# Performance work log

Hardware: AMD Instinct MI355X
Metric: run time of the kernel (lower is better)

Reference implementation:

```python
import jax, jax.numpy as jnp
import numpy as np

B, C, N = 8, 512, 8192
H = 8
D = C // H
HID = int(C * 2.0)
EPS_ATTN = 1e-6
EPS_BN = 1e-5


def setup_inputs() -> dict:
    key = jax.random.key(0)
    ks = jax.random.split(key, 8)
    sc = lambda fan_in: 1.0 / np.sqrt(fan_in)
    return {
        "x": jax.random.normal(ks[0], (B, C, N), dtype=jnp.float32),
        # qkv Linear: stored [in, out] for x @ W
        "qkv_w": jax.random.normal(ks[1], (C, 3 * C), dtype=jnp.float32) * sc(C),
        "qkv_b": jnp.zeros((3 * C,), dtype=jnp.float32),
        "proj_w": jax.random.normal(ks[2], (C, C), dtype=jnp.float32) * sc(C),
        "proj_b": jnp.zeros((C,), dtype=jnp.float32),
        # FFN conv1x1 (no bias, BN follows)
        "w1": jax.random.normal(ks[3], (HID, C), dtype=jnp.float32) * sc(C),
        "g1": jnp.ones((HID,), dtype=jnp.float32),
        "b1": jnp.zeros((HID,), dtype=jnp.float32),
        "w2": jax.random.normal(ks[4], (C, HID), dtype=jnp.float32) * sc(HID),
        "g2": jnp.ones((C,), dtype=jnp.float32),
        "b2": jnp.zeros((C,), dtype=jnp.float32),
    }


def _phi(x):
    # elu(x) + 1  (strictly positive kernel feature map)
    return jax.nn.elu(x) + 1.0


def _bn(x, gamma, beta):
    # training-mode BatchNorm1d over [B, C, N]: stats over (batch, spatial)
    mean = jnp.mean(x, axis=(0, 2), keepdims=True)
    var = jnp.var(x, axis=(0, 2), keepdims=True)
    xh = (x - mean) * jax.lax.rsqrt(var + EPS_BN)
    return xh * gamma[None, :, None] + beta[None, :, None]


def reference(x, qkv_w, qkv_b, proj_w, proj_b, w1, g1, b1, w2, g2, b2):
    # ---- linear attention ----
    xt = jnp.swapaxes(x, 1, 2)                       # [B, N, C]
    qkv = xt @ qkv_w + qkv_b                         # [B, N, 3C]
    q, k, v = jnp.split(qkv, 3, axis=-1)
    reshape_h = lambda t: jnp.swapaxes(t.reshape(B, N, H, D), 1, 2)  # [B, H, N, D]
    q, k, v = reshape_h(q), reshape_h(k), reshape_h(v)
    q_phi = _phi(q)
    k_phi = _phi(k)
    S = jnp.einsum("bhnd,bhne->bhde", k_phi, v)      # K^T V, [B,H,D,D]
    k_sum = k_phi.sum(axis=-2)                       # [B,H,D]
    numer = jnp.einsum("bhnd,bhde->bhne", q_phi, S)  # [B,H,N,D]
    denom = jnp.einsum("bhnd,bhd->bhn", q_phi, k_sum)[..., None] + EPS_ATTN
    out = numer / denom                              # [B,H,N,D]
    out = jnp.swapaxes(out, 1, 2).reshape(B, N, C)
    out = out @ proj_w + proj_b                      # [B, N, C]
    y = jnp.swapaxes(out, 1, 2)                      # [B, C, N]
    # ---- attention residual ----
    x = x + y
    # ---- FFN: conv1x1 -> BN -> ReLU, twice ----
    h = jnp.einsum("oc,bcn->bon", w1, x)             # [B, HID, N]
    h = jax.nn.relu(_bn(h, g1, b1))
    h = jnp.einsum("oc,bcn->bon", w2, h)             # [B, C, N]
    h = jax.nn.relu(_bn(h, g2, b2))
    return x + h
```

## Files before the change

kernel.cpp:

```cpp
#include <hip/hip_runtime.h>
#include <hip/hip_bf16.h>

#define B_    8
#define C_    512
#define N_    8192
#define H_    8
#define D_    64
#define HID_  1024

constexpr float EPS_ATTN = 1e-6f;
constexpr float EPS_BN   = 1e-5f;

typedef _Float16 half8 __attribute__((ext_vector_type(8)));
typedef _Float16 half4 __attribute__((ext_vector_type(4)));
typedef float    floatx4 __attribute__((ext_vector_type(4)));

#define GLOAD_LDS(gp, lp) \
  __builtin_amdgcn_global_load_lds((const __attribute__((address_space(1))) void*)(gp), \
                                   (__attribute__((address_space(3))) void*)(lp), 16, 0, 0)

template<int EPI>
__global__ __launch_bounds__(256)
void gemm_mfma(const _Float16* __restrict__ Abase, size_t a_bstride,
               const _Float16* __restrict__ Wt, int K,
               float* __restrict__ OUTf, size_t outf_bs,
               _Float16* __restrict__ OUTh, size_t outh_bs,
               const float* __restrict__ bias,
               const float* __restrict__ resid, size_t res_bs,
               int phi_limit)
{
    __shared__ _Float16 Al[4096];
    __shared__ _Float16 Bl[4096];

    const int tid = threadIdx.x;
    const int b = blockIdx.z;
    const int n_base = blockIdx.x * 128;
    const int o_base = blockIdx.y * 128;
    const int w = tid >> 6, l = tid & 63;
    const int wm = w >> 1, wn = w & 1;

    const _Float16* A  = Abase + (size_t)b * a_bstride + (size_t)n_base * K;
    const _Float16* Bw = Wt + (size_t)o_base * K;

    const int r0 = tid & 127;
    const int s0 = tid >> 7;
    const _Float16* ga0 = A  + (size_t)r0 * K + s0 * 8;
    const _Float16* ga1 = A  + (size_t)r0 * K + (2 + s0) * 8;
    const _Float16* gb0 = Bw + (size_t)r0 * K + s0 * 8;
    const _Float16* gb1 = Bw + (size_t)r0 * K + (2 + s0) * 8;
    _Float16* la0 = &Al[(size_t)(tid & 192) * 8];
    _Float16* la1 = &Al[(size_t)(256 + (tid & 192)) * 8];
    _Float16* lb0 = &Bl[(size_t)(tid & 192) * 8];
    _Float16* lb1 = &Bl[(size_t)(256 + (tid & 192)) * 8];

    floatx4 acc[4][4];
    #pragma unroll
    for (int mi = 0; mi < 4; ++mi)
        #pragma unroll
        for (int ni = 0; ni < 4; ++ni)
            acc[mi][ni] = (floatx4){0.f, 0.f, 0.f, 0.f};

    const int s = l >> 4;
    const int r = l & 15;

    for (int c0 = 0; c0 < K; c0 += 32) {
        GLOAD_LDS(ga0 + c0, la0);
        GLOAD_LDS(ga1 + c0, la1);
        GLOAD_LDS(gb0 + c0, lb0);
        GLOAD_LDS(gb1 + c0, lb1);
        __syncthreads();
        half8 af[4], bf[4];
        #pragma unroll
        for (int f = 0; f < 4; ++f) {
            af[f] = *(const half8*)&Al[(size_t)(s * 128 + wm * 64 + f * 16 + r) * 8];
            bf[f] = *(const half8*)&Bl[(size_t)(s * 128 + wn * 64 + f * 16 + r) * 8];
        }
        #pragma unroll
        for (int mi = 0; mi < 4; ++mi)
            #pragma unroll
            for (int ni = 0; ni < 4; ++ni)
                acc[mi][ni] = __builtin_amdgcn_mfma_f32_16x16x32_f16(af[mi], bf[ni], acc[mi][ni], 0, 0, 0);
        __syncthreads();
    }

    #pragma unroll
    for (int mi = 0; mi < 4; ++mi) {
        const int n_g = n_base + wm * 64 + mi * 16 + ((l >> 4) << 2);
        #pragma unroll
        for (int ni = 0; ni < 4; ++ni) {
            const int o_g = o_base + wn * 64 + ni * 16 + (l & 15);
            floatx4 v = acc[mi][ni];
            if (EPI == 1 || EPI == 2) {
                const float bi = bias[o_g];
                v[0] += bi; v[1] += bi; v[2] += bi; v[3] += bi;
            }
            if (EPI == 1) {
                if (o_g < phi_limit) {
                    #pragma unroll
                    for (int j = 0; j < 4; ++j)
                        v[j] = v[j] > 0.f ? v[j] + 1.f : __expf(v[j]);
                }
            }
            if (EPI == 2) {
                const float4 rv = *(const float4*)(resid + (size_t)b * res_bs + (size_t)o_g * N_ + n_g);
                v[0] += rv.x; v[1] += rv.y; v[2] += rv.z; v[3] += rv.w;
            }
            if (EPI == 0 || EPI == 1) {
                half4 hv;
                #pragma unroll
                for (int j = 0; j < 4; ++j) hv[j] = (_Float16)v[j];
                *(half4*)(OUTh + (size_t)b * outh_bs + (size_t)o_g * N_ + n_g) = hv;
            } else {
                *(floatx4*)(OUTf + (size_t)b * outf_bs + (size_t)o_g * N_ + n_g) = v;
            }
        }
    }
}

template<bool INF16, bool AFFINE>
__global__ __launch_bounds__(256)
void cvtT(const void* __restrict__ src, _Float16* __restrict__ dst,
          int R, int Cc, size_t sbs, size_t dbs,
          const float* __restrict__ scale, const float* __restrict__ shift)
{
    __shared__ _Float16 t[64][72];
    const int tid = threadIdx.x;
    const int b = blockIdx.z;
    const int c0 = blockIdx.x * 64;
    const int r0 = blockIdx.y * 64;
    const int rl = tid >> 3;
    const int cg = (tid & 7) * 8;
    #pragma unroll
    for (int hh = 0; hh < 2; ++hh) {
        const int rr = rl + hh * 32;
        float vals[8];
        if (INF16) {
            const _Float16* sp = (const _Float16*)src + (size_t)b * sbs + (size_t)(r0 + rr) * Cc + c0 + cg;
            const half8 hv = *(const half8*)sp;
            #pragma unroll
            for (int j = 0; j < 8; ++j) vals[j] = (float)hv[j];
        } else {
            const float* sp = (const float*)src + (size_t)b * sbs + (size_t)(r0 + rr) * Cc + c0 + cg;
            const float4 v0 = *(const float4*)sp;
            const float4 v1 = *(const float4*)(sp + 4);
            vals[0] = v0.x; vals[1] = v0.y; vals[2] = v0.z; vals[3] = v0.w;
            vals[4] = v1.x; vals[5] = v1.y; vals[6] = v1.z; vals[7] = v1.w;
        }
        if (AFFINE) {
            const float sc = scale[r0 + rr], sf = shift[r0 + rr];
            #pragma unroll
            for (int j = 0; j < 8; ++j) vals[j] = fmaxf(fmaf(vals[j], sc, sf), 0.f);
        }
        #pragma unroll
        for (int j = 0; j < 8; ++j) t[rr][cg + j] = (_Float16)vals[j];
    }
    __syncthreads();
    const int cl = tid >> 3;
    const int rg = (tid & 7) * 8;
    #pragma unroll
    for (int hh = 0; hh < 2; ++hh) {
        const int cc = cl + hh * 32;
        half8 o;
        #pragma unroll
        for (int j = 0; j < 8; ++j) o[j] = t[rg + j][cc];
        *(half8*)(dst + (size_t)b * dbs + (size_t)(c0 + cc) * R + r0 + rg) = o;
    }
}

__global__ __launch_bounds__(256)
void cast_f16(const float* __restrict__ in, _Float16* __restrict__ out, int n4)
{
    const int i = blockIdx.x * 256 + threadIdx.x;
    if (i < n4) {
        const float4 v = *(const float4*)(in + (size_t)i * 4);
        half4 h; h[0] = (_Float16)v.x; h[1] = (_Float16)v.y; h[2] = (_Float16)v.z; h[3] = (_Float16)v.w;
        *(half4*)(out + (size_t)i * 4) = h;
    }
}

__global__ __launch_bounds__(256)
void attn_kv_f16(const _Float16* __restrict__ qkvh, float* __restrict__ S, float* __restrict__ ksum)
{
    constexpr int TNK = 16;
    __shared__ float kt[64][17];
    __shared__ float vt[64][17];
    const int tid = threadIdx.x;
    const int bh = blockIdx.y;
    const int b = bh >> 3, h = bh & 7;
    const size_t kbase = ((size_t)b * 1536 + 512  + h * 64) * N_;
    const size_t vbase = ((size_t)b * 1536 + 1024 + h * 64) * N_;
    const int n0 = blockIdx.x * 1024;

    const int e  = tid & 63;
    const int dg = tid >> 6;
    float s[16];
    #pragma unroll
    for (int i = 0; i < 16; ++i) s[i] = 0.f;
    float ksl = 0.f;

    const int lr = tid >> 2;
    const int lc = (tid & 3) * 4;

    for (int it = 0; it < 1024 / TNK; ++it) {
        const int nt = n0 + it * TNK;
        const half4 k4 = *(const half4*)(qkvh + kbase + (size_t)lr * N_ + nt + lc);
        const half4 v4 = *(const half4*)(qkvh + vbase + (size_t)lr * N_ + nt + lc);
        __syncthreads();
        kt[lr][lc + 0] = (float)k4[0]; kt[lr][lc + 1] = (float)k4[1];
        kt[lr][lc + 2] = (float)k4[2]; kt[lr][lc + 3] = (float)k4[3];
        vt[lr][lc + 0] = (float)v4[0]; vt[lr][lc + 1] = (float)v4[1];
        vt[lr][lc + 2] = (float)v4[2]; vt[lr][lc + 3] = (float)v4[3];
        __syncthreads();
        if (tid < 64) {
            float kk = 0.f;
            #pragma unroll
            for (int nn = 0; nn < TNK; ++nn) kk += kt[tid][nn];
            ksl += kk;
        }
        #pragma unroll
        for (int nn = 0; nn < TNK; ++nn) {
            const float ve = vt[e][nn];
            #pragma unroll
            for (int i = 0; i < 16; ++i)
                s[i] = fmaf(kt[dg * 16 + i][nn], ve, s[i]);
        }
    }
    float* Sb = S + (size_t)bh * 64 * 64;
    #pragma unroll
    for (int i = 0; i < 16; ++i)
        atomicAdd(&Sb[(dg * 16 + i) * 64 + e], s[i]);
    if (tid < 64) atomicAdd(&ksum[bh * 64 + tid], ksl);
}

__global__ __launch_bounds__(256)
void attn_apply_f16(const _Float16* __restrict__ qkvh, const float* __restrict__ S,
                    const float* __restrict__ ksum, _Float16* __restrict__ attnb)
{
    const int tid = threadIdx.x;
    const int bh = blockIdx.y;
    const int b = bh >> 3, h = bh & 7;
    const int n = blockIdx.x * 256 + tid;
    const _Float16* __restrict__ qb = qkvh + ((size_t)b * 1536 + h * 64) * N_ + n;
    const float* __restrict__ Sb = S + (size_t)bh * 4096;
    const float* __restrict__ ks = ksum + bh * 64;
    float acc[64];
    #pragma unroll
    for (int e = 0; e < 64; ++e) acc[e] = 0.f;
    float den = EPS_ATTN;
    for (int d = 0; d < 64; ++d) {
        const float qd = (float)qb[(size_t)d * N_];
        den = fmaf(qd, ks[d], den);
        #pragma unroll
        for (int e = 0; e < 64; ++e)
            acc[e] = fmaf(qd, Sb[d * 64 + e], acc[e]);
    }
    const float inv = 1.0f / den;
    _Float16* __restrict__ ob = attnb + ((size_t)b * N_ + n) * C_ + h * 64;
    #pragma unroll
    for (int g = 0; g < 8; ++g) {
        half8 hv;
        #pragma unroll
        for (int j = 0; j < 8; ++j) hv[j] = (_Float16)(acc[g * 8 + j] * inv);
        *(half8*)(ob + g * 8) = hv;
    }
}

template<bool INF16>
__global__ __launch_bounds__(256)
void bn_stats(const void* __restrict__ X, size_t bstride,
              const float* __restrict__ gamma, const float* __restrict__ beta,
              float* __restrict__ scale, float* __restrict__ shift)
{
    const int ch = blockIdx.x;
    const int tid = threadIdx.x;
    double s = 0.0, s2 = 0.0;
    for (int b = 0; b < B_; ++b) {
        if (INF16) {
            const _Float16* base = (const _Float16*)X + (size_t)b * bstride + (size_t)ch * N_;
            for (int i = tid; i < N_ / 8; i += 256) {
                const half8 v = *(const half8*)(base + (size_t)i * 8);
                #pragma unroll
                for (int j = 0; j < 8; ++j) {
                    const float f = (float)v[j];
                    s += (double)f; s2 += (double)f * (double)f;
                }
            }
        } else {
            const float* base = (const float*)X + (size_t)b * bstride + (size_t)ch * N_;
            for (int i = tid; i < N_ / 4; i += 256) {
                const float4 v = *(const float4*)(base + (size_t)i * 4);
                s  += (double)v.x + (double)v.y + (double)v.z + (double)v.w;
                s2 += (double)v.x * v.x + (double)v.y * v.y + (double)v.z * v.z + (double)v.w * v.w;
            }
        }
    }
    __shared__ double sh[256], sh2[256];
    sh[tid] = s; sh2[tid] = s2;
    __syncthreads();
    for (int off = 128; off > 0; off >>= 1) {
        if (tid < off) { sh[tid] += sh[tid + off]; sh2[tid] += sh2[tid + off]; }
        __syncthreads();
    }
    if (tid == 0) {
        const double n = (double)B_ * (double)N_;
        const double mean = sh[0] / n;
        const double var  = sh2[0] / n - mean * mean;
        const double inv  = 1.0 / sqrt(var + (double)EPS_BN);
        const double g = (double)gamma[ch];
        scale[ch] = (float)(g * inv);
        shift[ch] = (float)((double)beta[ch] - mean * g * inv);
    }
}

__global__ __launch_bounds__(256)
void final_add(float* __restrict__ out, const float* __restrict__ h2,
               const float* __restrict__ scale, const float* __restrict__ shift)
{
    const size_t i = (size_t)blockIdx.x * 256 + threadIdx.x;
    const int c = (int)((i >> 11) & (C_ - 1));
    const float sc = scale[c], sf = shift[c];
    const float4 hv = ((const float4*)h2)[i];
    float4 xv = ((float4*)out)[i];
    xv.x += fmaxf(fmaf(hv.x, sc, sf), 0.f);
    xv.y += fmaxf(fmaf(hv.y, sc, sf), 0.f);
    xv.z += fmaxf(fmaf(hv.z, sc, sf), 0.f);
    xv.w += fmaxf(fmaf(hv.w, sc, sf), 0.f);
    ((float4*)out)[i] = xv;
}

extern "C" void kernel_launch(void* const* d_in, const int* in_sizes, int n_in,
                              void* d_out, int out_size, void* d_ws, size_t ws_size,
                              hipStream_t stream)
{
    const float* x      = (const float*)d_in[0];
    const float* qkv_w  = (const float*)d_in[1];
    const float* qkv_b  = (const float*)d_in[2];
    const float* proj_w = (const float*)d_in[3];
    const float* proj_b = (const float*)d_in[4];
    const float* w1     = (const float*)d_in[5];
    const float* g1     = (const float*)d_in[6];
    const float* b1     = (const float*)d_in[7];
    const float* w2     = (const float*)d_in[8];
    const float* g2     = (const float*)d_in[9];
    const float* b2     = (const float*)d_in[10];
    float* out = (float*)d_out;

    const size_t MB = 1ull << 20;
    char* ws = (char*)d_ws;
    _Float16* qkvh   = (_Float16*)ws;
    _Float16* h16    = (_Float16*)ws;
    float*    h2     = (float*)ws;
    _Float16* ht     = (_Float16*)(ws + 192 * MB);
    _Float16* xb     = (_Float16*)(ws + 320 * MB);
    _Float16* attnb  = xb;
    _Float16* x1b    = xb;
    _Float16* qkvwT  = (_Float16*)(ws + 384 * MB);
    _Float16* projwT = qkvwT + 1536 * 512;
    _Float16* w1h    = projwT + 512 * 512;
    _Float16* w2h    = w1h + 1024 * 512;
    float* S      = (float*)(ws + 390 * MB);
    float* ksum   = S + 262144;
    float* scale1 = ksum + 4096;
    float* shift1 = scale1 + 1024;
    float* scale2 = shift1 + 1024;
    float* shift2 = scale2 + 512;

    const size_t xbs = (size_t)C_ * N_;

    cvtT<false, false><<<dim3(24, 8, 1), 256, 0, stream>>>(qkv_w, qkvwT, 512, 1536, 0, 0, nullptr, nullptr);
    cvtT<false, false><<<dim3(8, 8, 1), 256, 0, stream>>>(proj_w, projwT, 512, 512, 0, 0, nullptr, nullptr);
    cast_f16<<<512, 256, 0, stream>>>(w1, w1h, 131072);
    cast_f16<<<512, 256, 0, stream>>>(w2, w2h, 131072);

    cvtT<false, false><<<dim3(128, 8, 8), 256, 0, stream>>>(x, xb, 512, 8192, xbs, (size_t)N_ * C_, nullptr, nullptr);

    hipMemsetAsync(S, 0, (262144 + 4096) * sizeof(float), stream);

    gemm_mfma<1><<<dim3(64, 12, 8), 256, 0, stream>>>(
        xb, (size_t)N_ * 512, qkvwT, 512,
        nullptr, 0, qkvh, (size_t)1536 * N_, qkv_b, nullptr, 0, 1024);

    attn_kv_f16<<<dim3(8, 64), 256, 0, stream>>>(qkvh, S, ksum);
    attn_apply_f16<<<dim3(32, 64), 256, 0, stream>>>(qkvh, S, ksum, attnb);

    gemm_mfma<2><<<dim3(64, 4, 8), 256, 0, stream>>>(
        attnb, (size_t)N_ * 512, projwT, 512,
        out, xbs, nullptr, 0, proj_b, x, xbs, 0);

    cvtT<false, false><<<dim3(128, 8, 8), 256, 0, stream>>>(out, x1b, 512, 8192, xbs, (size_t)N_ * C_, nullptr, nullptr);

    gemm_mfma<0><<<dim3(64, 8, 8), 256, 0, stream>>>(
        x1b, (size_t)N_ * 512, w1h, 512,
        nullptr, 0, h16, (size_t)HID_ * N_, nullptr, nullptr, 0, 0);

    bn_stats<true><<<1024, 256, 0, stream>>>(h16, (size_t)HID_ * N_, g1, b1, scale1, shift1);

    cvtT<true, true><<<dim3(128, 16, 8), 256, 0, stream>>>(
        h16, ht, 1024, 8192, (size_t)HID_ * N_, (size_t)N_ * HID_, scale1, shift1);

    gemm_mfma<3><<<dim3(64, 4, 8), 256, 0, stream>>>(
        ht, (size_t)N_ * 1024, w2h, 1024,
        h2, xbs, nullptr, 0, nullptr, nullptr, 0, 0);

    bn_stats<false><<<512, 256, 0, stream>>>(h2, xbs, g2, b2, scale2, shift2);

    final_add<<<32768, 256, 0, stream>>>(out, h2, scale2, shift2);
}
```

Baseline: 1.323 ms.

## Double-buffer GEMM LDS, MFMA-based KV reduction, fp16 second FFN output

```diff
diff --git a/kernel.cpp b/kernel.cpp
--- a/kernel.cpp
+++ b/kernel.cpp
@@ -29,8 +29,8 @@
                const float* __restrict__ resid, size_t res_bs,
                int phi_limit)
 {
-    __shared__ _Float16 Al[4096];
-    __shared__ _Float16 Bl[4096];
+    __shared__ _Float16 Al0[4096], Al1[4096];
+    __shared__ _Float16 Bl0[4096], Bl1[4096];
 
     const int tid = threadIdx.x;
     const int b = blockIdx.z;
@@ -48,10 +48,7 @@
     const _Float16* ga1 = A  + (size_t)r0 * K + (2 + s0) * 8;
     const _Float16* gb0 = Bw + (size_t)r0 * K + s0 * 8;
     const _Float16* gb1 = Bw + (size_t)r0 * K + (2 + s0) * 8;
-    _Float16* la0 = &Al[(size_t)(tid & 192) * 8];
-    _Float16* la1 = &Al[(size_t)(256 + (tid & 192)) * 8];
-    _Float16* lb0 = &Bl[(size_t)(tid & 192) * 8];
-    _Float16* lb1 = &Bl[(size_t)(256 + (tid & 192)) * 8];
+    const int loff = (tid & 192) * 8;
 
     floatx4 acc[4][4];
     #pragma unroll
@@ -63,23 +60,35 @@
     const int s = l >> 4;
     const int r = l & 15;
 
-    for (int c0 = 0; c0 < K; c0 += 32) {
-        GLOAD_LDS(ga0 + c0, la0);
-        GLOAD_LDS(ga1 + c0, la1);
-        GLOAD_LDS(gb0 + c0, lb0);
-        GLOAD_LDS(gb1 + c0, lb1);
-        __syncthreads();
+    auto stage = [&](_Float16* AlB, _Float16* BlB, int c0) {
+        GLOAD_LDS(ga0 + c0, AlB + loff);
+        GLOAD_LDS(ga1 + c0, AlB + 2048 + loff);
+        GLOAD_LDS(gb0 + c0, BlB + loff);
+        GLOAD_LDS(gb1 + c0, BlB + 2048 + loff);
+    };
+    auto compute = [&](const _Float16* AlB, const _Float16* BlB) {
         half8 af[4], bf[4];
         #pragma unroll
         for (int f = 0; f < 4; ++f) {
-            af[f] = *(const half8*)&Al[(size_t)(s * 128 + wm * 64 + f * 16 + r) * 8];
-            bf[f] = *(const half8*)&Bl[(size_t)(s * 128 + wn * 64 + f * 16 + r) * 8];
+            af[f] = *(const half8*)&AlB[(size_t)(s * 128 + wm * 64 + f * 16 + r) * 8];
+            bf[f] = *(const half8*)&BlB[(size_t)(s * 128 + wn * 64 + f * 16 + r) * 8];
         }
         #pragma unroll
         for (int mi = 0; mi < 4; ++mi)
             #pragma unroll
             for (int ni = 0; ni < 4; ++ni)
                 acc[mi][ni] = __builtin_amdgcn_mfma_f32_16x16x32_f16(af[mi], bf[ni], acc[mi][ni], 0, 0, 0);
+    };
+
+    const int NT = K >> 5;
+    stage(Al0, Bl0, 0);
+    __syncthreads();
+    for (int t = 0; t < NT; t += 2) {
+        stage(Al1, Bl1, (t + 1) << 5);
+        compute(Al0, Bl0);
+        __syncthreads();
+        if (t + 2 < NT) stage(Al0, Bl0, (t + 2) << 5);
+        compute(Al1, Bl1);
         __syncthreads();
     }
 
@@ -104,14 +113,12 @@
             if (EPI == 2) {
                 const float4 rv = *(const float4*)(resid + (size_t)b * res_bs + (size_t)o_g * N_ + n_g);
                 v[0] += rv.x; v[1] += rv.y; v[2] += rv.z; v[3] += rv.w;
-            }
-            if (EPI == 0 || EPI == 1) {
+                *(floatx4*)(OUTf + (size_t)b * outf_bs + (size_t)o_g * N_ + n_g) = v;
+            } else {
                 half4 hv;
                 #pragma unroll
                 for (int j = 0; j < 4; ++j) hv[j] = (_Float16)v[j];
                 *(half4*)(OUTh + (size_t)b * outh_bs + (size_t)o_g * N_ + n_g) = hv;
-            } else {
-                *(floatx4*)(OUTf + (size_t)b * outf_bs + (size_t)o_g * N_ + n_g) = v;
             }
         }
     }
@@ -123,7 +130,7 @@
           int R, int Cc, size_t sbs, size_t dbs,
           const float* __restrict__ scale, const float* __restrict__ shift)
 {
-    __shared__ _Float16 t[64][72];
+    __shared__ _Float16 t[64][76];
     const int tid = threadIdx.x;
     const int b = blockIdx.z;
     const int c0 = blockIdx.x * 64;
@@ -179,57 +186,92 @@
 }
 
 __global__ __launch_bounds__(256)
-void attn_kv_f16(const _Float16* __restrict__ qkvh, float* __restrict__ S, float* __restrict__ ksum)
-{
-    constexpr int TNK = 16;
-    __shared__ float kt[64][17];
-    __shared__ float vt[64][17];
+void attn_kv_mfma(const _Float16* __restrict__ qkvh,
+                  float* __restrict__ S_part, float* __restrict__ ks_part)
+{
+    __shared__ _Float16 kt0[2048], kt1[2048], vt0[2048], vt1[2048];
     const int tid = threadIdx.x;
     const int bh = blockIdx.y;
     const int b = bh >> 3, h = bh & 7;
     const size_t kbase = ((size_t)b * 1536 + 512  + h * 64) * N_;
     const size_t vbase = ((size_t)b * 1536 + 1024 + h * 64) * N_;
     const int n0 = blockIdx.x * 1024;
-
-    const int e  = tid & 63;
-    const int dg = tid >> 6;
-    float s[16];
-    #pragma unroll
-    for (int i = 0; i < 16; ++i) s[i] = 0.f;
-    float ksl = 0.f;
-
-    const int lr = tid >> 2;
-    const int lc = (tid & 3) * 4;
-
-    for (int it = 0; it < 1024 / TNK; ++it) {
-        const int nt = n0 + it * TNK;
-        const half4 k4 = *(const half4*)(qkvh + kbase + (size_t)lr * N_ + nt + lc);
-        const half4 v4 = *(const half4*)(qkvh + vbase + (size_t)lr * N_ + nt + lc);
+    const int w = tid >> 6, l = tid & 63;
+
+    const int rr = tid & 63, ss = tid >> 6;
+    const _Float16* gk = qkvh + kbase + (size_t)rr * N_ + n0 + ss * 8;
+    const _Float16* gv = qkvh + vbase + (size_t)rr * N_ + n0 + ss * 8;
+    const int loff = (tid & 192) * 8;
+
+    floatx4 acc[4], accks;
+    #pragma unroll
+    for (int ni = 0; ni < 4; ++ni) acc[ni] = (floatx4){0.f, 0.f, 0.f, 0.f};
+    accks = (floatx4){0.f, 0.f, 0.f, 0.f};
+
+    const int s = l >> 4, r = l & 15;
+    const int drow = w * 16 + r;
+    half8 onesv;
+    #pragma unroll
+    for (int j = 0; j < 8; ++j) onesv[j] = (_Float16)1.0f;
+
+    auto stage = [&](_Float16* kB, _Float16* vB, int nt) {
+        GLOAD_LDS(gk + nt, kB + loff);
+        GLOAD_LDS(gv + nt, vB + loff);
+    };
+    auto compute = [&](const _Float16* kB, const _Float16* vB) {
+        const half8 af = *(const half8*)&kB[(size_t)(s * 64 + drow) * 8];
+        half8 bf[4];
+        #pragma unroll
+        for (int ni = 0; ni < 4; ++ni)
+            bf[ni] = *(const half8*)&vB[(size_t)(s * 64 + ni * 16 + r) * 8];
+        #pragma unroll
+        for (int ni = 0; ni < 4; ++ni)
+            acc[ni] = __builtin_amdgcn_mfma_f32_16x16x32_f16(af, bf[ni], acc[ni], 0, 0, 0);
+        accks = __builtin_amdgcn_mfma_f32_16x16x32_f16(af, onesv, accks, 0, 0, 0);
+    };
+
+    stage(kt0, vt0, 0);
+    __syncthreads();
+    for (int t = 0; t < 32; t += 2) {
+        stage(kt1, vt1, (t + 1) * 32);
+        compute(kt0, vt0);
         __syncthreads();
-        kt[lr][lc + 0] = (float)k4[0]; kt[lr][lc + 1] = (float)k4[1];
-        kt[lr][lc + 2] = (float)k4[2]; kt[lr][lc + 3] = (float)k4[3];
-        vt[lr][lc + 0] = (float)v4[0]; vt[lr][lc + 1] = (float)v4[1];
-        vt[lr][lc + 2] = (float)v4[2]; vt[lr][lc + 3] = (float)v4[3];
+        if (t + 2 < 32) stage(kt0, vt0, (t + 2) * 32);
+        compute(kt1, vt1);
         __syncthreads();
-        if (tid < 64) {
-            float kk = 0.f;
-            #pragma unroll
-            for (int nn = 0; nn < TNK; ++nn) kk += kt[tid][nn];
-            ksl += kk;
-        }
-        #pragma unroll
-        for (int nn = 0; nn < TNK; ++nn) {
-            const float ve = vt[e][nn];
-            #pragma unroll
-            for (int i = 0; i < 16; ++i)
-                s[i] = fmaf(kt[dg * 16 + i][nn], ve, s[i]);
-        }
-    }
-    float* Sb = S + (size_t)bh * 64 * 64;
-    #pragma unroll
-    for (int i = 0; i < 16; ++i)
-        atomicAdd(&Sb[(dg * 16 + i) * 64 + e], s[i]);
-    if (tid < 64) atomicAdd(&ksum[bh * 64 + tid], ksl);
+    }
+
+    float* Sp = S_part + ((size_t)blockIdx.x * 64 + bh) * 4096;
+    #pragma unroll
+    for (int ni = 0; ni < 4; ++ni)
+        #pragma unroll
+        for (int j = 0; j < 4; ++j)
+            Sp[(w * 16 + s * 4 + j) * 64 + ni * 16 + r] = acc[ni][j];
+    if (r == 0) {
+        float* kp = ks_part + ((size_t)blockIdx.x * 64 + bh) * 64;
+        #pragma unroll
+        for (int j = 0; j < 4; ++j) kp[w * 16 + s * 4 + j] = accks[j];
+    }
+}
+
+__global__ __launch_bounds__(256)
+void attn_reduce(const float* __restrict__ S_part, const float* __restrict__ ks_part,
+                 float* __restrict__ S, float* __restrict__ ksum)
+{
+    const int bh = blockIdx.x;
+    const int tid = threadIdx.x;
+    for (int i = tid; i < 4096; i += 256) {
+        float s = 0.f;
+        #pragma unroll
+        for (int c = 0; c < 8; ++c) s += S_part[((size_t)c * 64 + bh) * 4096 + i];
+        S[(size_t)bh * 4096 + i] = s;
+    }
+    if (tid < 64) {
+        float s = 0.f;
+        #pragma unroll
+        for (int c = 0; c < 8; ++c) s += ks_part[((size_t)c * 64 + bh) * 64 + tid];
+        ksum[bh * 64 + tid] = s;
+    }
 }
 
 __global__ __launch_bounds__(256)
@@ -265,32 +307,22 @@
     }
 }
 
-template<bool INF16>
-__global__ __launch_bounds__(256)
-void bn_stats(const void* __restrict__ X, size_t bstride,
-              const float* __restrict__ gamma, const float* __restrict__ beta,
-              float* __restrict__ scale, float* __restrict__ shift)
+__global__ __launch_bounds__(256)
+void bn_stats_h(const _Float16* __restrict__ X, size_t bstride,
+                const float* __restrict__ gamma, const float* __restrict__ beta,
+                float* __restrict__ scale, float* __restrict__ shift)
 {
     const int ch = blockIdx.x;
     const int tid = threadIdx.x;
     double s = 0.0, s2 = 0.0;
     for (int b = 0; b < B_; ++b) {
-        if (INF16) {
-            const _Float16* base = (const _Float16*)X + (size_t)b * bstride + (size_t)ch * N_;
-            for (int i = tid; i < N_ / 8; i += 256) {
-                const half8 v = *(const half8*)(base + (size_t)i * 8);
-                #pragma unroll
-                for (int j = 0; j < 8; ++j) {
-                    const float f = (float)v[j];
-                    s += (double)f; s2 += (double)f * (double)f;
-                }
-            }
-        } else {
-            const float* base = (const float*)X + (size_t)b * bstride + (size_t)ch * N_;
-            for (int i = tid; i < N_ / 4; i += 256) {
-                const float4 v = *(const float4*)(base + (size_t)i * 4);
-                s  += (double)v.x + (double)v.y + (double)v.z + (double)v.w;
-                s2 += (double)v.x * v.x + (double)v.y * v.y + (double)v.z * v.z + (double)v.w * v.w;
+        const _Float16* base = X + (size_t)b * bstride + (size_t)ch * N_;
+        for (int i = tid; i < N_ / 8; i += 256) {
+            const half8 v = *(const half8*)(base + (size_t)i * 8);
+            #pragma unroll
+            for (int j = 0; j < 8; ++j) {
+                const float f = (float)v[j];
+                s += (double)f; s2 += (double)f * (double)f;
             }
         }
     }
@@ -313,19 +345,25 @@
 }
 
 __global__ __launch_bounds__(256)
-void final_add(float* __restrict__ out, const float* __restrict__ h2,
-               const float* __restrict__ scale, const float* __restrict__ shift)
+void final_add_h(float* __restrict__ out, const _Float16* __restrict__ h2,
+                 const float* __restrict__ scale, const float* __restrict__ shift)
 {
     const size_t i = (size_t)blockIdx.x * 256 + threadIdx.x;
-    const int c = (int)((i >> 11) & (C_ - 1));
+    const int c = (int)((i >> 10) & (C_ - 1));
     const float sc = scale[c], sf = shift[c];
-    const float4 hv = ((const float4*)h2)[i];
-    float4 xv = ((float4*)out)[i];
-    xv.x += fmaxf(fmaf(hv.x, sc, sf), 0.f);
-    xv.y += fmaxf(fmaf(hv.y, sc, sf), 0.f);
-    xv.z += fmaxf(fmaf(hv.z, sc, sf), 0.f);
-    xv.w += fmaxf(fmaf(hv.w, sc, sf), 0.f);
-    ((float4*)out)[i] = xv;
+    const half8 hv = *(const half8*)(h2 + i * 8);
+    float4 x0 = ((float4*)out)[i * 2];
+    float4 x1 = ((float4*)out)[i * 2 + 1];
+    x0.x += fmaxf(fmaf((float)hv[0], sc, sf), 0.f);
+    x0.y += fmaxf(fmaf((float)hv[1], sc, sf), 0.f);
+    x0.z += fmaxf(fmaf((float)hv[2], sc, sf), 0.f);
+    x0.w += fmaxf(fmaf((float)hv[3], sc, sf), 0.f);
+    x1.x += fmaxf(fmaf((float)hv[4], sc, sf), 0.f);
+    x1.y += fmaxf(fmaf((float)hv[5], sc, sf), 0.f);
+    x1.z += fmaxf(fmaf((float)hv[6], sc, sf), 0.f);
+    x1.w += fmaxf(fmaf((float)hv[7], sc, sf), 0.f);
+    ((float4*)out)[i * 2] = x0;
+    ((float4*)out)[i * 2 + 1] = x1;
 }
 
 extern "C" void kernel_launch(void* const* d_in, const int* in_sizes, int n_in,
@@ -349,7 +387,11 @@
     char* ws = (char*)d_ws;
     _Float16* qkvh   = (_Float16*)ws;
     _Float16* h16    = (_Float16*)ws;
-    float*    h2     = (float*)ws;
+    _Float16* h2h    = (_Float16*)(ws + 128 * MB);
+    float*    S_part = (float*)(ws + 192 * MB);
+    float*    ks_part= (float*)(ws + 200 * MB);
+    float*    S      = (float*)(ws + 201 * MB);
+    float*    ksum   = (float*)(ws + 202 * MB);
     _Float16* ht     = (_Float16*)(ws + 192 * MB);
     _Float16* xb     = (_Float16*)(ws + 320 * MB);
     _Float16* attnb  = xb;
@@ -358,9 +400,7 @@
     _Float16* projwT = qkvwT + 1536 * 512;
     _Float16* w1h    = projwT + 512 * 512;
     _Float16* w2h    = w1h + 1024 * 512;
-    float* S      = (float*)(ws + 390 * MB);
-    float* ksum   = S + 262144;
-    float* scale1 = ksum + 4096;
+    float* scale1 = (float*)(w2h + 512 * 1024);
     float* shift1 = scale1 + 1024;
     float* scale2 = shift1 + 1024;
     float* shift2 = scale2 + 512;
@@ -374,13 +414,12 @@
 
     cvtT<false, false><<<dim3(128, 8, 8), 256, 0, stream>>>(x, xb, 512, 8192, xbs, (size_t)N_ * C_, nullptr, nullptr);
 
-    hipMemsetAsync(S, 0, (262144 + 4096) * sizeof(float), stream);
-
     gemm_mfma<1><<<dim3(64, 12, 8), 256, 0, stream>>>(
         xb, (size_t)N_ * 512, qkvwT, 512,
         nullptr, 0, qkvh, (size_t)1536 * N_, qkv_b, nullptr, 0, 1024);
 
-    attn_kv_f16<<<dim3(8, 64), 256, 0, stream>>>(qkvh, S, ksum);
+    attn_kv_mfma<<<dim3(8, 64), 256, 0, stream>>>(qkvh, S_part, ks_part);
+    attn_reduce<<<64, 256, 0, stream>>>(S_part, ks_part, S, ksum);
     attn_apply_f16<<<dim3(32, 64), 256, 0, stream>>>(qkvh, S, ksum, attnb);
 
     gemm_mfma<2><<<dim3(64, 4, 8), 256, 0, stream>>>(
@@ -393,16 +432,16 @@
         x1b, (size_t)N_ * 512, w1h, 512,
         nullptr, 0, h16, (size_t)HID_ * N_, nullptr, nullptr, 0, 0);
 
-    bn_stats<true><<<1024, 256, 0, stream>>>(h16, (size_t)HID_ * N_, g1, b1, scale1, shift1);
+    bn_stats_h<<<1024, 256, 0, stream>>>(h16, (size_t)HID_ * N_, g1, b1, scale1, shift1);
 
     cvtT<true, true><<<dim3(128, 16, 8), 256, 0, stream>>>(
         h16, ht, 1024, 8192, (size_t)HID_ * N_, (size_t)N_ * HID_, scale1, shift1);
 
-    gemm_mfma<3><<<dim3(64, 4, 8), 256, 0, stream>>>(
+    gemm_mfma<0><<<dim3(64, 4, 8), 256, 0, stream>>>(
         ht, (size_t)N_ * 1024, w2h, 1024,
-        h2, xbs, nullptr, 0, nullptr, nullptr, 0, 0);
-
-    bn_stats<false><<<512, 256, 0, stream>>>(h2, xbs, g2, b2, scale2, shift2);
-
-    final_add<<<32768, 256, 0, stream>>>(out, h2, scale2, shift2);
-}
+        nullptr, 0, h2h, xbs, nullptr, nullptr, 0, 0);
+
+    bn_stats_h<<<512, 256, 0, stream>>>(h2h, xbs, g2, b2, scale2, shift2);
+
+    final_add_h<<<16384, 256, 0, stream>>>(out, h2h, scale2, shift2);
+}
```

New measurement: 1.173 ms. 11.4% less time.
